# Kernel optimization log

Hardware: AMD Instinct MI355X
Metric: run time of the kernel (lower is better)

## Reference

```python
import jax, jax.numpy as jnp
import numpy as np

B, H, W = 4, 64, 64
INPLANES, PLANES, G, K = 608, 152, 19, 3
KK = K * K
EPS = 1e-5


def conv2d(x, w, stride=1, padding=0, dilation=1):
    return jax.lax.conv_general_dilated(
        x, w, (stride, stride), [(padding, padding)] * 2,
        rhs_dilation=(dilation, dilation),
        dimension_numbers=("NCHW", "OIHW", "NCHW"))


def bn(x, g, b, m, v):
    # inference-mode batchnorm (affine with running stats)
    inv = g / jnp.sqrt(v + EPS)
    return x * inv[None, :, None, None] + (b - m * inv)[None, :, None, None]


def deform_conv(x, offset, w, pad=1, dil=1):
    # x: [B,C,H,W], offset: [B, 2*G*KK, H, W] ((dy,dx) pairs per group per tap), w: [Cout,C,K,K]
    Bs, C, Hh, Ww = x.shape
    Cg = C // G
    off = offset.reshape(Bs, G, KK, 2, Hh, Ww)
    ky, kx = jnp.meshgrid(jnp.arange(K), jnp.arange(K), indexing="ij")
    base_y = (jnp.arange(Hh) - pad)[None, None, None, :, None] + (dil * ky.reshape(-1))[None, None, :, None, None]
    base_x = (jnp.arange(Ww) - pad)[None, None, None, None, :] + (dil * kx.reshape(-1))[None, None, :, None, None]
    ys = base_y + off[:, :, :, 0]  # [B,G,KK,H,W]
    xs = base_x + off[:, :, :, 1]
    y0 = jnp.floor(ys)
    x0 = jnp.floor(xs)
    wy = ys - y0
    wx = xs - x0
    y0i = y0.astype(jnp.int32)
    x0i = x0.astype(jnp.int32)
    xf = x.reshape(Bs, G, Cg, Hh * Ww)

    def gather(yi, xi, wgt):
        valid = ((yi >= 0) & (yi < Hh) & (xi >= 0) & (xi < Ww)).astype(x.dtype)
        idx = jnp.clip(yi, 0, Hh - 1) * Ww + jnp.clip(xi, 0, Ww - 1)
        idxf = jnp.broadcast_to(idx.reshape(Bs, G, 1, KK * Hh * Ww), (Bs, G, Cg, KK * Hh * Ww))
        g = jnp.take_along_axis(xf, idxf, axis=3).reshape(Bs, G, Cg, KK, Hh, Ww)
        return g * (wgt * valid)[:, :, None]

    samp = (gather(y0i, x0i, (1 - wy) * (1 - wx))
            + gather(y0i, x0i + 1, (1 - wy) * wx)
            + gather(y0i + 1, x0i, wy * (1 - wx))
            + gather(y0i + 1, x0i + 1, wy * wx))  # [B,G,Cg,KK,H,W]
    wr = w.reshape(w.shape[0], G, Cg, KK)
    return jnp.einsum("bgckhw,ogck->bohw", samp, wr)


def setup_inputs() -> dict:
    key = jax.random.key(0)
    ks = jax.random.split(key, 8)
    d = {}
    d["x"] = jax.random.normal(ks[0], (B, INPLANES, H, W), jnp.float32)
    d["conv1_w"] = jax.random.normal(ks[1], (PLANES, INPLANES, 1, 1), jnp.float32) * 0.05
    d["conv2_w"] = jax.random.normal(ks[2], (2 * G * KK, PLANES, 3, 3), jnp.float32) * 0.01
    d["dconv_w"] = jax.random.normal(ks[3], (PLANES, PLANES, 3, 3), jnp.float32) * 0.05
    d["conv3_w"] = jax.random.normal(ks[4], (4 * PLANES, PLANES, 1, 1), jnp.float32) * 0.05
    for i, (name, c) in enumerate([("bn1", PLANES), ("bn2", PLANES), ("bn3", 4 * PLANES)]):
        k1, k2, k3, k4 = jax.random.split(ks[5 + i], 4)
        d[name + "_g"] = jax.random.uniform(k1, (c,), jnp.float32, 0.5, 1.5)
        d[name + "_b"] = jax.random.normal(k2, (c,), jnp.float32) * 0.1
        d[name + "_m"] = jax.random.normal(k3, (c,), jnp.float32) * 0.1
        d[name + "_v"] = jax.random.uniform(k4, (c,), jnp.float32, 0.5, 1.5)
    return d


def reference(x, conv1_w, conv2_w, dconv_w, conv3_w,
              bn1_g, bn1_b, bn1_m, bn1_v,
              bn2_g, bn2_b, bn2_m, bn2_v,
              bn3_g, bn3_b, bn3_m, bn3_v):
    out = jax.nn.relu(conv2d(x, conv1_w))           # conv1 -> relu (order as in source)
    out = bn(out, bn1_g, bn1_b, bn1_m, bn1_v)       # -> bn1
    offset = conv2d(out, conv2_w, padding=1)         # offset-generating 3x3 conv
    out = deform_conv(out, offset, dconv_w)          # deformable 3x3 conv
    out = bn(jax.nn.relu(out), bn2_g, bn2_b, bn2_m, bn2_v)
    out = bn(conv2d(out, conv3_w), bn3_g, bn3_b, bn3_m, bn3_v)
    return jax.nn.relu(out + x)
```

## Files before the change

### kernel.cpp

```cpp
#include <hip/hip_runtime.h>

#define EPSV 1e-5f

typedef __bf16 bf16_t;
typedef __bf16 bf16x8 __attribute__((ext_vector_type(8)));
typedef float f32x4 __attribute__((ext_vector_type(4)));

__device__ inline bf16x8 bzero8() {
  bf16x8 z;
#pragma unroll
  for (int i = 0; i < 8; i++) z[i] = (bf16_t)0.f;
  return z;
}

__device__ inline f32x4 mfma16(bf16x8 a, bf16x8 b, f32x4 c) {
  return __builtin_amdgcn_mfma_f32_16x16x32_bf16(a, b, c, 0, 0, 0);
}

#define W1E (160 * 608)
#define W2E (384 * 1376)
#define WDE (192 * 1440)
#define W3E (640 * 160)

__global__ __launch_bounds__(256) void prep_weights(
    const float* __restrict__ w1, const float* __restrict__ w2,
    const float* __restrict__ wd, const float* __restrict__ w3,
    bf16_t* __restrict__ w1b, bf16_t* __restrict__ w2b,
    bf16_t* __restrict__ wdb, bf16_t* __restrict__ w3b) {
  int i = blockIdx.x * 256 + threadIdx.x;
  float v = 0.f;
  if (i < W1E) {
    int oc = i / 608, ic = i % 608;
    if (oc < 152) v = w1[oc * 608 + ic];
    w1b[i] = (bf16_t)v;
  } else if (i < W1E + W2E) {
    int j = i - W1E;
    int oc = j / 1376, k = j % 1376;
    if (oc < 342 && k < 1368) {
      int t = k / 152, ic = k % 152;
      v = w2[(oc * 152 + ic) * 9 + t];
    }
    w2b[j] = (bf16_t)v;
  } else if (i < W1E + W2E + WDE) {
    int j = i - W1E - W2E;
    int o = j / 1440, k = j % 1440;
    int t = k / 160, ic = k % 160;
    if (o < 152 && ic < 152) v = wd[(o * 152 + ic) * 9 + t];
    wdb[j] = (bf16_t)v;
  } else if (i < W1E + W2E + WDE + W3E) {
    int j = i - W1E - W2E - WDE;
    int oc = j / 160, ic = j % 160;
    if (oc < 608 && ic < 152) v = w3[oc * 152 + ic];
    w3b[j] = (bf16_t)v;
  }
}

__global__ void prep_bn(const float* g1, const float* b1, const float* m1, const float* v1,
                        const float* g2, const float* b2, const float* m2, const float* v2,
                        const float* g3, const float* b3, const float* m3, const float* v3,
                        float* __restrict__ bnc) {
  int i = threadIdx.x;
  if (i < 152) {
    float inv = g1[i] / sqrtf(v1[i] + EPSV);
    bnc[i] = inv;
    bnc[152 + i] = b1[i] - m1[i] * inv;
    float inv2 = g2[i] / sqrtf(v2[i] + EPSV);
    bnc[304 + i] = inv2;
    bnc[456 + i] = b2[i] - m2[i] * inv2;
  }
  if (i < 608) {
    float inv3 = g3[i] / sqrtf(v3[i] + EPSV);
    bnc[608 + i] = inv3;
    bnc[1216 + i] = b3[i] - m3[i] * inv3;
  }
}

__global__ __launch_bounds__(256) void s1_conv1(const float* __restrict__ x,
                                                const bf16_t* __restrict__ w1b,
                                                const float* __restrict__ bnc,
                                                bf16_t* __restrict__ out1) {
  __shared__ bf16_t t1[32 * 616];
  int tid = threadIdx.x;
  int px0 = blockIdx.x * 32;
  int b = px0 >> 12, sp0 = px0 & 4095;
  for (int task = tid; task < 608 * 8; task += 256) {
    int c = task >> 3, i4 = task & 7;
    f32x4 v = *(const f32x4*)(x + (((size_t)(b * 608 + c)) << 12) + sp0 + i4 * 4);
#pragma unroll
    for (int i = 0; i < 4; i++) t1[(i4 * 4 + i) * 616 + c] = (bf16_t)v[i];
  }
  __syncthreads();
  int wid = tid >> 6, lane = tid & 63, q = lane >> 4, lr = lane & 15;
  int mw = wid & 1, nw = wid >> 1;
  f32x4 acc[5];
#pragma unroll
  for (int n = 0; n < 5; n++) acc[n] = (f32x4){0.f, 0.f, 0.f, 0.f};
  for (int kk = 0; kk < 19; kk++) {
    int k0 = kk * 32 + q * 8;
    bf16x8 a = *(const bf16x8*)(t1 + (mw * 16 + lr) * 616 + k0);
#pragma unroll
    for (int n = 0; n < 5; n++) {
      bf16x8 bf = *(const bf16x8*)(w1b + (nw * 80 + n * 16 + lr) * 608 + k0);
      acc[n] = mfma16(a, bf, acc[n]);
    }
  }
#pragma unroll
  for (int n = 0; n < 5; n++) {
    int oc = nw * 80 + n * 16 + lr;
    if (oc < 152) {
      float inv = bnc[oc], beta = bnc[152 + oc];
#pragma unroll
      for (int i = 0; i < 4; i++) {
        int p = px0 + mw * 16 + q * 4 + i;
        float v = fmaxf(acc[n][i], 0.f) * inv + beta;
        out1[(size_t)p * 152 + oc] = (bf16_t)v;
      }
    }
  }
}

__global__ __launch_bounds__(256, 4) void s2_offs(const bf16_t* __restrict__ out1,
                                                  const bf16_t* __restrict__ w2b,
                                                  float* __restrict__ offs) {
  __shared__ bf16_t t2[3 * 34 * 156];
  int tid = threadIdx.x;
  int nh = blockIdx.x & 1;
  int rest = blockIdx.x >> 1;
  int xh = rest & 1, y = (rest >> 1) & 63, b = rest >> 7;
  const bf16_t* ob = out1 + (((size_t)b) << 12) * 152;
  int x0 = xh * 32 - 1;
  for (int task = tid; task < 3 * 34 * 19; task += 256) {
    int j = task / 646, r = task % 646;
    int xi = r / 19, cb = r % 19;
    int yy = y + j - 1, xx = x0 + xi;
    bf16x8 v = bzero8();
    if (yy >= 0 && yy < 64 && xx >= 0 && xx < 64)
      v = *(const bf16x8*)(ob + (size_t)(yy * 64 + xx) * 152 + cb * 8);
    *(bf16x8*)(t2 + (j * 34 + xi) * 156 + cb * 8) = v;
  }
  __syncthreads();
  int wid = tid >> 6, lane = tid & 63, q = lane >> 4, lr = lane & 15;
  int ncol0 = nh * 192 + wid * 48;
  f32x4 acc[2][3];
#pragma unroll
  for (int m = 0; m < 2; m++)
#pragma unroll
    for (int n = 0; n < 3; n++) acc[m][n] = (f32x4){0.f, 0.f, 0.f, 0.f};
  const bf16_t* wb = w2b + (size_t)(ncol0 + lr) * 1376;
#pragma unroll
  for (int kk = 0; kk < 43; kk++) {
    int k0 = kk * 32 + q * 8;
    bf16x8 bfr[3];
#pragma unroll
    for (int n = 0; n < 3; n++)
      bfr[n] = *(const bf16x8*)(wb + (size_t)(n * 16) * 1376 + k0);
    bf16x8 a[2];
    if (k0 < 1368) {
      int t = k0 / 152, c0 = k0 - t * 152;
      int dy = t / 3, dxp1 = t - dy * 3;
#pragma unroll
      for (int m = 0; m < 2; m++)
        a[m] = *(const bf16x8*)(t2 + (dy * 34 + m * 16 + lr + dxp1) * 156 + c0);
    } else {
      a[0] = bzero8();
      a[1] = bzero8();
    }
#pragma unroll
    for (int n = 0; n < 3; n++)
#pragma unroll
      for (int m = 0; m < 2; m++) acc[m][n] = mfma16(a[m], bfr[n], acc[m][n]);
  }
#pragma unroll
  for (int n = 0; n < 3; n++) {
    int col = ncol0 + n * 16 + lr;
    if (col < 342) {
#pragma unroll
      for (int m = 0; m < 2; m++)
#pragma unroll
        for (int i = 0; i < 4; i++) {
          int p = (b << 12) + y * 64 + xh * 32 + m * 16 + q * 4 + i;
          offs[(size_t)p * 344 + col] = acc[m][n][i];
        }
    }
  }
}

__global__ __launch_bounds__(256, 8) void s3a_sample(const bf16_t* __restrict__ out1,
                                                     const float* __restrict__ offs,
                                                     bf16_t* __restrict__ samp) {
  int task = blockIdx.x * 256 + threadIdx.x;
  int lp = task / 171, s = task - lp * 171;
  int t = s / 19, g = s - t * 19;
  int b = lp >> 12, y = (lp >> 6) & 63, xc = lp & 63;
  int ky = t / 3, kx = t - ky * 3;
  float2 ov = *(const float2*)(offs + (size_t)lp * 344 + g * 18 + t * 2);
  float ys = (float)(y - 1 + ky) + ov.x;
  float xs = (float)(xc - 1 + kx) + ov.y;
  float y0f = floorf(ys), x0f = floorf(xs);
  float wy = ys - y0f, wx = xs - x0f;
  int y0 = (int)y0f, x0 = (int)x0f;
  int y1 = y0 + 1, x1 = x0 + 1;
  int y0c = min(max(y0, 0), 63), x0c = min(max(x0, 0), 63);
  int y1c = min(max(y1, 0), 63), x1c = min(max(x1, 0), 63);
  float vy0 = (y0 == y0c) ? 1.f : 0.f;
  float vy1 = (y1 == y1c) ? 1.f : 0.f;
  float vx0 = (x0 == x0c) ? 1.f : 0.f;
  float vx1 = (x1 == x1c) ? 1.f : 0.f;
  float w00 = (1.f - wy) * (1.f - wx) * vy0 * vx0;
  float w01 = (1.f - wy) * wx * vy0 * vx1;
  float w10 = wy * (1.f - wx) * vy1 * vx0;
  float w11 = wy * wx * vy1 * vx1;
  const bf16_t* bg = out1 + (((size_t)b << 12) * 152) + g * 8;
  bf16x8 c00 = *(const bf16x8*)(bg + (size_t)(y0c * 64 + x0c) * 152);
  bf16x8 c01 = *(const bf16x8*)(bg + (size_t)(y0c * 64 + x1c) * 152);
  bf16x8 c10 = *(const bf16x8*)(bg + (size_t)(y1c * 64 + x0c) * 152);
  bf16x8 c11 = *(const bf16x8*)(bg + (size_t)(y1c * 64 + x1c) * 152);
  bf16x8 o;
#pragma unroll
  for (int i = 0; i < 8; i++) {
    float f = w00 * (float)c00[i];
    f = fmaf(w01, (float)c01[i], f);
    f = fmaf(w10, (float)c10[i], f);
    f = fmaf(w11, (float)c11[i], f);
    o[i] = (bf16_t)f;
  }
  *(bf16x8*)(samp + (size_t)lp * 1440 + t * 160 + g * 8) = o;
  if (g == 18) *(bf16x8*)(samp + (size_t)lp * 1440 + t * 160 + 152) = bzero8();
}

__global__ __launch_bounds__(256, 4) void s3b_gemm(const bf16_t* __restrict__ samp,
                                                   const bf16_t* __restrict__ wdb,
                                                   const float* __restrict__ bnc,
                                                   bf16_t* __restrict__ a2) {
  __shared__ bf16_t at[2][32 * 168];
  int tid = threadIdx.x;
  int row0 = blockIdx.x * 32;
  int wid = tid >> 6, lane = tid & 63, q = lane >> 4, lr = lane & 15;
  f32x4 acc[2][3];
#pragma unroll
  for (int m = 0; m < 2; m++)
#pragma unroll
    for (int n = 0; n < 3; n++) acc[m][n] = (f32x4){0.f, 0.f, 0.f, 0.f};
  const bf16_t* wb = wdb + (size_t)(wid * 48 + lr) * 1440;
  const bf16_t* arow = samp + (size_t)row0 * 1440;

#define STAGE(T, BUF)                                                        \
  for (int task = tid; task < 640; task += 256) {                            \
    int r = task / 20, c8 = task - r * 20;                                   \
    *(bf16x8*)(at[BUF] + r * 168 + c8 * 8) =                                 \
        *(const bf16x8*)(arow + (size_t)r * 1440 + (T)*160 + c8 * 8);        \
  }

#define TAP(T, BUF)                                                          \
  {                                                                          \
    if ((T) < 8) STAGE((T) + 1, (BUF) ^ 1)                                   \
    _Pragma("unroll") for (int kk = 0; kk < 5; kk++) {                       \
      int k0 = kk * 32 + q * 8;                                              \
      bf16x8 a0 = *(const bf16x8*)(at[BUF] + lr * 168 + k0);                 \
      bf16x8 a1 = *(const bf16x8*)(at[BUF] + (16 + lr) * 168 + k0);          \
      _Pragma("unroll") for (int n = 0; n < 3; n++) {                        \
        bf16x8 bf =                                                          \
            *(const bf16x8*)(wb + (size_t)(n * 16) * 1440 + (T)*160 + k0);   \
        acc[0][n] = mfma16(a0, bf, acc[0][n]);                               \
        acc[1][n] = mfma16(a1, bf, acc[1][n]);                               \
      }                                                                      \
    }                                                                        \
    __syncthreads();                                                         \
  }

  STAGE(0, 0)
  __syncthreads();
  TAP(0, 0)
  TAP(1, 1)
  TAP(2, 0)
  TAP(3, 1)
  TAP(4, 0)
  TAP(5, 1)
  TAP(6, 0)
  TAP(7, 1)
  TAP(8, 0)
#undef TAP
#undef STAGE

#pragma unroll
  for (int n = 0; n < 3; n++) {
    int oc = wid * 48 + n * 16 + lr;
    if (oc < 152) {
      float inv = bnc[304 + oc], beta = bnc[456 + oc];
#pragma unroll
      for (int m = 0; m < 2; m++)
#pragma unroll
        for (int i = 0; i < 4; i++) {
          int p = row0 + m * 16 + q * 4 + i;
          float v = fmaxf(acc[m][n][i], 0.f) * inv + beta;
          a2[(size_t)p * 152 + oc] = (bf16_t)v;
        }
    }
  }
}

__global__ __launch_bounds__(256) void s4_conv3(const bf16_t* __restrict__ a2,
                                                const bf16_t* __restrict__ w3b,
                                                const float* __restrict__ bnc,
                                                const float* __restrict__ x,
                                                float* __restrict__ out) {
  int tid = threadIdx.x;
  int wid = tid >> 6, lane = tid & 63, q = lane >> 4, lr = lane & 15;
  int p0 = blockIdx.x * 16;
  int b = p0 >> 12, sp0 = p0 & 4095;
  f32x4 acc[10];
#pragma unroll
  for (int n = 0; n < 10; n++) acc[n] = (f32x4){0.f, 0.f, 0.f, 0.f};
  for (int kk = 0; kk < 5; kk++) {
    int k0 = kk * 32 + q * 8;
    bf16x8 a = (k0 < 152) ? *(const bf16x8*)(a2 + (size_t)(p0 + lr) * 152 + k0) : bzero8();
#pragma unroll
    for (int n = 0; n < 10; n++) {
      bf16x8 bf = *(const bf16x8*)(w3b + (size_t)(wid * 160 + n * 16 + lr) * 160 + k0);
      acc[n] = mfma16(a, bf, acc[n]);
    }
  }
#pragma unroll
  for (int n = 0; n < 10; n++) {
    int oc = wid * 160 + n * 16 + lr;
    if (oc < 608) {
      float inv = bnc[608 + oc], beta = bnc[1216 + oc];
      size_t gi = (((size_t)(b * 608 + oc)) << 12) + sp0 + q * 4;
      f32x4 xr = *(const f32x4*)(x + gi);
      f32x4 o;
#pragma unroll
      for (int i = 0; i < 4; i++) o[i] = fmaxf(acc[n][i] * inv + beta + xr[i], 0.f);
      *(f32x4*)(out + gi) = o;
    }
  }
}

extern "C" void kernel_launch(void* const* d_in, const int* in_sizes, int n_in,
                              void* d_out, int out_size, void* d_ws, size_t ws_size,
                              hipStream_t stream) {
  const float* x = (const float*)d_in[0];
  const float* w1 = (const float*)d_in[1];
  const float* w2 = (const float*)d_in[2];
  const float* wd = (const float*)d_in[3];
  const float* w3 = (const float*)d_in[4];
  const float* g1 = (const float*)d_in[5];
  const float* b1 = (const float*)d_in[6];
  const float* m1 = (const float*)d_in[7];
  const float* v1 = (const float*)d_in[8];
  const float* g2 = (const float*)d_in[9];
  const float* b2 = (const float*)d_in[10];
  const float* m2 = (const float*)d_in[11];
  const float* v2 = (const float*)d_in[12];
  const float* g3 = (const float*)d_in[13];
  const float* b3 = (const float*)d_in[14];
  const float* m3 = (const float*)d_in[15];
  const float* v3 = (const float*)d_in[16];

  char* ws = (char*)d_ws;
  bf16_t* w1b = (bf16_t*)(ws + 0);
  bf16_t* w2b = (bf16_t*)(ws + 194560);
  bf16_t* wdb = (bf16_t*)(ws + 1251328);
  bf16_t* w3b = (bf16_t*)(ws + 1804288);
  float* bnc = (float*)(ws + 2009088);
  bf16_t* out1 = (bf16_t*)(ws + 2016384);
  float* offs = (float*)(ws + 6997120);
  bf16_t* samp = (bf16_t*)(ws + 29541504);
  bf16_t* a2 = (bf16_t*)(ws + 2016384);
  float* out = (float*)d_out;

  prep_weights<<<3924, 256, 0, stream>>>(w1, w2, wd, w3, w1b, w2b, wdb, w3b);
  prep_bn<<<1, 640, 0, stream>>>(g1, b1, m1, v1, g2, b2, m2, v2, g3, b3, m3, v3, bnc);
  s1_conv1<<<512, 256, 0, stream>>>(x, w1b, bnc, out1);
  s2_offs<<<1024, 256, 0, stream>>>(out1, w2b, offs);
  s3a_sample<<<10944, 256, 0, stream>>>(out1, offs, samp);
  s3b_gemm<<<512, 256, 0, stream>>>(samp, wdb, bnc, a2);
  s4_conv3<<<1024, 256, 0, stream>>>(a2, w3b, bnc, x, out);
}
```

Measured before the change: 180.1 us.

## Use zero-padded activation buffer and direct global-to-LDS loads in offset and deform GEMMs

```diff
diff --git a/kernel.cpp b/kernel.cpp
--- a/kernel.cpp
+++ b/kernel.cpp
@@ -6,6 +6,11 @@
 typedef __bf16 bf16x8 __attribute__((ext_vector_type(8)));
 typedef float f32x4 __attribute__((ext_vector_type(4)));
 
+#define GLOAD_LDS(g, l)                                             \
+  __builtin_amdgcn_global_load_lds(                                 \
+      (const __attribute__((address_space(1))) void*)(g),           \
+      (__attribute__((address_space(3))) void*)(l), 16, 0, 0)
+
 __device__ inline bf16x8 bzero8() {
   bf16x8 z;
 #pragma unroll
@@ -18,7 +23,7 @@
 }
 
 #define W1E (160 * 608)
-#define W2E (384 * 1376)
+#define W2E (384 * 1440)
 #define WDE (192 * 1440)
 #define W3E (640 * 160)
 
@@ -35,11 +40,9 @@
     w1b[i] = (bf16_t)v;
   } else if (i < W1E + W2E) {
     int j = i - W1E;
-    int oc = j / 1376, k = j % 1376;
-    if (oc < 342 && k < 1368) {
-      int t = k / 152, ic = k % 152;
-      v = w2[(oc * 152 + ic) * 9 + t];
-    }
+    int oc = j / 1440, k = j % 1440;
+    int t = k / 160, ic = k % 160;
+    if (oc < 342 && ic < 152) v = w2[(oc * 152 + ic) * 9 + t];
     w2b[j] = (bf16_t)v;
   } else if (i < W1E + W2E + WDE) {
     int j = i - W1E - W2E;
@@ -78,7 +81,7 @@
 __global__ __launch_bounds__(256) void s1_conv1(const float* __restrict__ x,
                                                 const bf16_t* __restrict__ w1b,
                                                 const float* __restrict__ bnc,
-                                                bf16_t* __restrict__ out1) {
+                                                bf16_t* __restrict__ out1p) {
   __shared__ bf16_t t1[32 * 616];
   int tid = threadIdx.x;
   int px0 = blockIdx.x * 32;
@@ -112,80 +115,98 @@
 #pragma unroll
       for (int i = 0; i < 4; i++) {
         int p = px0 + mw * 16 + q * 4 + i;
+        int y = (p >> 6) & 63, xx = p & 63;
         float v = fmaxf(acc[n][i], 0.f) * inv + beta;
-        out1[(size_t)p * 152 + oc] = (bf16_t)v;
+        out1p[(size_t)(b * 4356 + (y + 1) * 66 + (xx + 1)) * 152 + oc] = (bf16_t)v;
       }
     }
   }
 }
 
-__global__ __launch_bounds__(256, 4) void s2_offs(const bf16_t* __restrict__ out1,
+__global__ __launch_bounds__(256, 4) void s2_offs(const bf16_t* __restrict__ out1p,
                                                   const bf16_t* __restrict__ w2b,
+                                                  const bf16_t* __restrict__ zbuf,
                                                   float* __restrict__ offs) {
-  __shared__ bf16_t t2[3 * 34 * 156];
+  __shared__ bf16_t At[2][128 * 32];
+  __shared__ bf16_t Bt[2][96 * 32];
   int tid = threadIdx.x;
-  int nh = blockIdx.x & 1;
-  int rest = blockIdx.x >> 1;
-  int xh = rest & 1, y = (rest >> 1) & 63, b = rest >> 7;
-  const bf16_t* ob = out1 + (((size_t)b) << 12) * 152;
-  int x0 = xh * 32 - 1;
-  for (int task = tid; task < 3 * 34 * 19; task += 256) {
-    int j = task / 646, r = task % 646;
-    int xi = r / 19, cb = r % 19;
-    int yy = y + j - 1, xx = x0 + xi;
-    bf16x8 v = bzero8();
-    if (yy >= 0 && yy < 64 && xx >= 0 && xx < 64)
-      v = *(const bf16x8*)(ob + (size_t)(yy * 64 + xx) * 152 + cb * 8);
-    *(bf16x8*)(t2 + (j * 34 + xi) * 156 + cb * 8) = v;
-  }
+  int w = tid >> 6, l = tid & 63;
+  int ct = blockIdx.x & 3;
+  int p0 = (blockIdx.x >> 2) * 128;
+  int c0 = ct * 96;
+  int lr = l & 15, q = l >> 4;
+  int mw = w & 1, nw = w >> 1;
+  int rA = l >> 2, cA = l & 3;
+  int b = p0 >> 12;
+
+  f32x4 acc[4][3];
+#pragma unroll
+  for (int m = 0; m < 4; m++)
+#pragma unroll
+    for (int n = 0; n < 3; n++) acc[m][n] = (f32x4){0.f, 0.f, 0.f, 0.f};
+
+#define S2_STAGE(KK, BUF)                                                      \
+  {                                                                            \
+    int kk_ = (KK);                                                            \
+    int t_ = kk_ / 5;                                                          \
+    int ic0_ = (kk_ - t_ * 5) * 32;                                            \
+    int dy_ = t_ / 3 - 1, dx_ = t_ - (t_ / 3) * 3 - 1;                         \
+    int doff_ = dy_ * 66 + dx_;                                                \
+    int ic_ = ic0_ + cA * 8;                                                   \
+    for (int s = w; s < 8; s += 4) {                                           \
+      int px = p0 + s * 16 + rA;                                               \
+      int y = (px >> 6) & 63, xx = px & 63;                                    \
+      const bf16_t* g =                                                        \
+          (ic_ < 152)                                                          \
+              ? out1p + (size_t)(b * 4356 + (y + 1) * 66 + (xx + 1) + doff_) * \
+                            152 +                                              \
+                    ic_                                                        \
+              : zbuf + cA * 8;                                                 \
+      GLOAD_LDS(g, &At[BUF][s * 512]);                                         \
+    }                                                                          \
+    for (int s = w; s < 6; s += 4) {                                           \
+      int col = c0 + s * 16 + rA;                                              \
+      const bf16_t* g = w2b + (size_t)col * 1440 + kk_ * 32 + cA * 8;          \
+      GLOAD_LDS(g, &Bt[BUF][s * 512]);                                         \
+    }                                                                          \
+  }
+
+  S2_STAGE(0, 0)
   __syncthreads();
-  int wid = tid >> 6, lane = tid & 63, q = lane >> 4, lr = lane & 15;
-  int ncol0 = nh * 192 + wid * 48;
-  f32x4 acc[2][3];
-#pragma unroll
-  for (int m = 0; m < 2; m++)
-#pragma unroll
-    for (int n = 0; n < 3; n++) acc[m][n] = (f32x4){0.f, 0.f, 0.f, 0.f};
-  const bf16_t* wb = w2b + (size_t)(ncol0 + lr) * 1376;
-#pragma unroll
-  for (int kk = 0; kk < 43; kk++) {
-    int k0 = kk * 32 + q * 8;
-    bf16x8 bfr[3];
+  for (int kk = 0; kk < 45; kk++) {
+    int buf = kk & 1;
+    if (kk < 44) S2_STAGE(kk + 1, buf ^ 1)
+    bf16x8 a[4], bfr[3];
+#pragma unroll
+    for (int m = 0; m < 4; m++)
+      a[m] = *(const bf16x8*)&At[buf][(mw * 64 + m * 16 + lr) * 32 + q * 8];
 #pragma unroll
     for (int n = 0; n < 3; n++)
-      bfr[n] = *(const bf16x8*)(wb + (size_t)(n * 16) * 1376 + k0);
-    bf16x8 a[2];
-    if (k0 < 1368) {
-      int t = k0 / 152, c0 = k0 - t * 152;
-      int dy = t / 3, dxp1 = t - dy * 3;
-#pragma unroll
-      for (int m = 0; m < 2; m++)
-        a[m] = *(const bf16x8*)(t2 + (dy * 34 + m * 16 + lr + dxp1) * 156 + c0);
-    } else {
-      a[0] = bzero8();
-      a[1] = bzero8();
-    }
-#pragma unroll
-    for (int n = 0; n < 3; n++)
-#pragma unroll
-      for (int m = 0; m < 2; m++) acc[m][n] = mfma16(a[m], bfr[n], acc[m][n]);
-  }
+      bfr[n] = *(const bf16x8*)&Bt[buf][(nw * 48 + n * 16 + lr) * 32 + q * 8];
+#pragma unroll
+    for (int m = 0; m < 4; m++)
+#pragma unroll
+      for (int n = 0; n < 3; n++) acc[m][n] = mfma16(a[m], bfr[n], acc[m][n]);
+    __syncthreads();
+  }
+#undef S2_STAGE
+
 #pragma unroll
   for (int n = 0; n < 3; n++) {
-    int col = ncol0 + n * 16 + lr;
+    int col = c0 + nw * 48 + n * 16 + lr;
     if (col < 342) {
 #pragma unroll
-      for (int m = 0; m < 2; m++)
+      for (int m = 0; m < 4; m++)
 #pragma unroll
         for (int i = 0; i < 4; i++) {
-          int p = (b << 12) + y * 64 + xh * 32 + m * 16 + q * 4 + i;
-          offs[(size_t)p * 344 + col] = acc[m][n][i];
+          int px = p0 + mw * 64 + m * 16 + q * 4 + i;
+          offs[(size_t)px * 344 + col] = acc[m][n][i];
         }
     }
   }
 }
 
-__global__ __launch_bounds__(256, 8) void s3a_sample(const bf16_t* __restrict__ out1,
+__global__ __launch_bounds__(256, 8) void s3a_sample(const bf16_t* __restrict__ out1p,
                                                      const float* __restrict__ offs,
                                                      bf16_t* __restrict__ samp) {
   int task = blockIdx.x * 256 + threadIdx.x;
@@ -210,11 +231,11 @@
   float w01 = (1.f - wy) * wx * vy0 * vx1;
   float w10 = wy * (1.f - wx) * vy1 * vx0;
   float w11 = wy * wx * vy1 * vx1;
-  const bf16_t* bg = out1 + (((size_t)b << 12) * 152) + g * 8;
-  bf16x8 c00 = *(const bf16x8*)(bg + (size_t)(y0c * 64 + x0c) * 152);
-  bf16x8 c01 = *(const bf16x8*)(bg + (size_t)(y0c * 64 + x1c) * 152);
-  bf16x8 c10 = *(const bf16x8*)(bg + (size_t)(y1c * 64 + x0c) * 152);
-  bf16x8 c11 = *(const bf16x8*)(bg + (size_t)(y1c * 64 + x1c) * 152);
+  const bf16_t* bg = out1p + (size_t)(b * 4356) * 152 + g * 8;
+  bf16x8 c00 = *(const bf16x8*)(bg + (size_t)((y0c + 1) * 66 + x0c + 1) * 152);
+  bf16x8 c01 = *(const bf16x8*)(bg + (size_t)((y0c + 1) * 66 + x1c + 1) * 152);
+  bf16x8 c10 = *(const bf16x8*)(bg + (size_t)((y1c + 1) * 66 + x0c + 1) * 152);
+  bf16x8 c11 = *(const bf16x8*)(bg + (size_t)((y1c + 1) * 66 + x1c + 1) * 152);
   bf16x8 o;
 #pragma unroll
   for (int i = 0; i < 8; i++) {
@@ -232,68 +253,69 @@
                                                    const bf16_t* __restrict__ wdb,
                                                    const float* __restrict__ bnc,
                                                    bf16_t* __restrict__ a2) {
-  __shared__ bf16_t at[2][32 * 168];
+  __shared__ bf16_t At[2][64 * 32];
+  __shared__ bf16_t Bt[2][96 * 32];
   int tid = threadIdx.x;
-  int row0 = blockIdx.x * 32;
-  int wid = tid >> 6, lane = tid & 63, q = lane >> 4, lr = lane & 15;
+  int w = tid >> 6, l = tid & 63;
+  int c0 = (blockIdx.x & 1) * 96;
+  int p0 = (blockIdx.x >> 1) * 64;
+  int lr = l & 15, q = l >> 4;
+  int mw = w & 1, nw = w >> 1;
+  int rA = l >> 2, cA = l & 3;
+
   f32x4 acc[2][3];
 #pragma unroll
   for (int m = 0; m < 2; m++)
 #pragma unroll
     for (int n = 0; n < 3; n++) acc[m][n] = (f32x4){0.f, 0.f, 0.f, 0.f};
-  const bf16_t* wb = wdb + (size_t)(wid * 48 + lr) * 1440;
-  const bf16_t* arow = samp + (size_t)row0 * 1440;
-
-#define STAGE(T, BUF)                                                        \
-  for (int task = tid; task < 640; task += 256) {                            \
-    int r = task / 20, c8 = task - r * 20;                                   \
-    *(bf16x8*)(at[BUF] + r * 168 + c8 * 8) =                                 \
-        *(const bf16x8*)(arow + (size_t)r * 1440 + (T)*160 + c8 * 8);        \
-  }
-
-#define TAP(T, BUF)                                                          \
-  {                                                                          \
-    if ((T) < 8) STAGE((T) + 1, (BUF) ^ 1)                                   \
-    _Pragma("unroll") for (int kk = 0; kk < 5; kk++) {                       \
-      int k0 = kk * 32 + q * 8;                                              \
-      bf16x8 a0 = *(const bf16x8*)(at[BUF] + lr * 168 + k0);                 \
-      bf16x8 a1 = *(const bf16x8*)(at[BUF] + (16 + lr) * 168 + k0);          \
-      _Pragma("unroll") for (int n = 0; n < 3; n++) {                        \
-        bf16x8 bf =                                                          \
-            *(const bf16x8*)(wb + (size_t)(n * 16) * 1440 + (T)*160 + k0);   \
-        acc[0][n] = mfma16(a0, bf, acc[0][n]);                               \
-        acc[1][n] = mfma16(a1, bf, acc[1][n]);                               \
-      }                                                                      \
-    }                                                                        \
-    __syncthreads();                                                         \
-  }
-
-  STAGE(0, 0)
+
+#define S3_STAGE(KK, BUF)                                                     \
+  {                                                                           \
+    int kk_ = (KK);                                                           \
+    for (int s = w; s < 4; s += 4) {                                          \
+      int px = p0 + s * 16 + rA;                                              \
+      const bf16_t* g = samp + (size_t)px * 1440 + kk_ * 32 + cA * 8;         \
+      GLOAD_LDS(g, &At[BUF][s * 512]);                                        \
+    }                                                                         \
+    for (int s = w; s < 6; s += 4) {                                          \
+      int col = c0 + s * 16 + rA;                                             \
+      const bf16_t* g = wdb + (size_t)col * 1440 + kk_ * 32 + cA * 8;         \
+      GLOAD_LDS(g, &Bt[BUF][s * 512]);                                        \
+    }                                                                         \
+  }
+
+  S3_STAGE(0, 0)
   __syncthreads();
-  TAP(0, 0)
-  TAP(1, 1)
-  TAP(2, 0)
-  TAP(3, 1)
-  TAP(4, 0)
-  TAP(5, 1)
-  TAP(6, 0)
-  TAP(7, 1)
-  TAP(8, 0)
-#undef TAP
-#undef STAGE
+  for (int kk = 0; kk < 45; kk++) {
+    int buf = kk & 1;
+    if (kk < 44) S3_STAGE(kk + 1, buf ^ 1)
+    bf16x8 a[2], bfr[3];
+#pragma unroll
+    for (int m = 0; m < 2; m++)
+      a[m] = *(const bf16x8*)&At[buf][(mw * 32 + m * 16 + lr) * 32 + q * 8];
+#pragma unroll
+    for (int n = 0; n < 3; n++)
+      bfr[n] = *(const bf16x8*)&Bt[buf][(nw * 48 + n * 16 + lr) * 32 + q * 8];
+#pragma unroll
+    for (int m = 0; m < 2; m++)
+#pragma unroll
+      for (int n = 0; n < 3; n++) acc[m][n] = mfma16(a[m], bfr[n], acc[m][n]);
+    __syncthreads();
+  }
+#undef S3_STAGE
 
 #pragma unroll
   for (int n = 0; n < 3; n++) {
-    int oc = wid * 48 + n * 16 + lr;
+    int oc = c0 + nw * 48 + n * 16 + lr;
     if (oc < 152) {
       float inv = bnc[304 + oc], beta = bnc[456 + oc];
 #pragma unroll
       for (int m = 0; m < 2; m++)
 #pragma unroll
         for (int i = 0; i < 4; i++) {
-          int p = row0 + m * 16 + q * 4 + i;
+          int px = p0 + mw * 32 + m * 16 + q * 4 + i;
           float v = fmaxf(acc[m][n][i], 0.f) * inv + beta;
-          a2[(size_t)p * 152 + oc] = (bf16_t)v;
+          a2[(size_t)px * 152 + oc] = (bf16_t)v;
         }
     }
   }
@@ -359,20 +381,23 @@
   char* ws = (char*)d_ws;
   bf16_t* w1b = (bf16_t*)(ws + 0);
   bf16_t* w2b = (bf16_t*)(ws + 194560);
-  bf16_t* wdb = (bf16_t*)(ws + 1251328);
-  bf16_t* w3b = (bf16_t*)(ws + 1804288);
-  float* bnc = (float*)(ws + 2009088);
-  bf16_t* out1 = (bf16_t*)(ws + 2016384);
-  float* offs = (float*)(ws + 6997120);
-  bf16_t* samp = (bf16_t*)(ws + 29541504);
-  bf16_t* a2 = (bf16_t*)(ws + 2016384);
+  bf16_t* wdb = (bf16_t*)(ws + 1300480);
+  bf16_t* w3b = (bf16_t*)(ws + 1853440);
+  float* bnc = (float*)(ws + 2058240);
+  bf16_t* zbuf = (bf16_t*)(ws + 2065536);
+  bf16_t* out1p = (bf16_t*)(ws + 2065600);
+  float* offs = (float*)(ws + 7363264);
+  bf16_t* samp = (bf16_t*)(ws + 29907648);
+  bf16_t* a2 = (bf16_t*)(ws + 2065600);
   float* out = (float*)d_out;
 
-  prep_weights<<<3924, 256, 0, stream>>>(w1, w2, wd, w3, w1b, w2b, wdb, w3b);
+  hipMemsetAsync(ws + 2065536, 0, 64 + 5297664, stream);
+
+  prep_weights<<<4020, 256, 0, stream>>>(w1, w2, wd, w3, w1b, w2b, wdb, w3b);
   prep_bn<<<1, 640, 0, stream>>>(g1, b1, m1, v1, g2, b2, m2, v2, g3, b3, m3, v3, bnc);
-  s1_conv1<<<512, 256, 0, stream>>>(x, w1b, bnc, out1);
-  s2_offs<<<1024, 256, 0, stream>>>(out1, w2b, offs);
-  s3a_sample<<<10944, 256, 0, stream>>>(out1, offs, samp);
+  s1_conv1<<<512, 256, 0, stream>>>(x, w1b, bnc, out1p);
+  s2_offs<<<512, 256, 0, stream>>>(out1p, w2b, zbuf, offs);
+  s3a_sample<<<10944, 256, 0, stream>>>(out1p, offs, samp);
   s3b_gemm<<<512, 256, 0, stream>>>(samp, wdb, bnc, a2);
   s4_conv3<<<1024, 256, 0, stream>>>(a2, w3b, bnc, x, out);
 }
```

After: 166.7 us. 7.5% less time.
